# Performance work log

Hardware: AMD Instinct MI355X
Metric: run time of the kernel (lower is better)

## Reference

```python
import jax, jax.numpy as jnp
import numpy as np

NB_CAT = 8192       # nb_category per column
RANK = 16           # low-rank factor dimension
N_COLS = 4          # number of categorical columns (len(embedding_sizes))
N_PAIRS = 1048576   # number of (x, y) index pairs
FRAC_DIAG = 0.9     # fraction_diagonal init


def setup_inputs() -> dict:
    key = jax.random.key(0)
    k1, k2, k3, k4 = jax.random.split(key, 4)
    x = jax.random.randint(k1, (N_PAIRS, N_COLS), 0, NB_CAT, dtype=jnp.int32)
    y = jax.random.randint(k2, (N_PAIRS, N_COLS), 0, NB_CAT, dtype=jnp.int32)
    # params initialized as in the torch module, plus small noise so values are non-degenerate
    std = (FRAC_DIAG * jnp.ones((N_COLS, NB_CAT), dtype=jnp.float32)
           + 0.01 * jax.random.normal(k3, (N_COLS, NB_CAT), dtype=jnp.float32))
    covar_factor = ((1.0 - FRAC_DIAG) / np.float32(np.sqrt(RANK))
                    * jnp.ones((N_COLS, NB_CAT, RANK), dtype=jnp.float32)
                    + 0.01 * jax.random.normal(k4, (N_COLS, NB_CAT, RANK), dtype=jnp.float32))
    return {"x": x, "y": y, "covar_factor": covar_factor, "std": std}


def reference(x, y, covar_factor, std):
    # Build full covariance per column: F @ F.T + diag(std^2)   -> [C, N, N]
    cov = jnp.einsum('cnr,cmr->cnm', covar_factor, covar_factor)
    diag_idx = jnp.arange(cov.shape[1])
    cov = cov.at[:, diag_idx, diag_idx].add(std * std)
    # Gather requested (x, y) entries per column, then reduce (should_reduce=True)
    cols = jnp.arange(cov.shape[0])  # [C]
    vals = cov[cols[None, :], x, y]  # [B, C]
    return vals.sum(axis=-1)         # [B]
```

## Files before the change

### kernel.cpp

```cpp
#include <hip/hip_runtime.h>

#define NB_CAT  8192
#define RANK    16
#define N_COLS  4
#define N_PAIRS 1048576

#define SLICES      (N_COLS * 2)
#define SLICE_ROWS  NB_CAT
#define SLICE_BYTES (SLICE_ROWS * 16)
#define TBL_BYTES   ((size_t)SLICES * SLICE_BYTES)

typedef _Float16 half2_t __attribute__((ext_vector_type(2)));

#if defined(__has_builtin)
#if __has_builtin(__builtin_amdgcn_fdot2)
#define HAVE_FDOT2 1
#endif
#endif

__device__ __forceinline__ float dot8_f16(uint4 A, uint4 B, float acc) {
#ifdef HAVE_FDOT2
    acc = __builtin_amdgcn_fdot2(__builtin_bit_cast(half2_t, A.x), __builtin_bit_cast(half2_t, B.x), acc, false);
    acc = __builtin_amdgcn_fdot2(__builtin_bit_cast(half2_t, A.y), __builtin_bit_cast(half2_t, B.y), acc, false);
    acc = __builtin_amdgcn_fdot2(__builtin_bit_cast(half2_t, A.z), __builtin_bit_cast(half2_t, B.z), acc, false);
    acc = __builtin_amdgcn_fdot2(__builtin_bit_cast(half2_t, A.w), __builtin_bit_cast(half2_t, B.w), acc, false);
#else
    half2_t ax = __builtin_bit_cast(half2_t, A.x), bx = __builtin_bit_cast(half2_t, B.x);
    half2_t ay = __builtin_bit_cast(half2_t, A.y), by = __builtin_bit_cast(half2_t, B.y);
    half2_t az = __builtin_bit_cast(half2_t, A.z), bz = __builtin_bit_cast(half2_t, B.z);
    half2_t aw = __builtin_bit_cast(half2_t, A.w), bw = __builtin_bit_cast(half2_t, B.w);
    acc = fmaf((float)ax[0], (float)bx[0], acc); acc = fmaf((float)ax[1], (float)bx[1], acc);
    acc = fmaf((float)ay[0], (float)by[0], acc); acc = fmaf((float)ay[1], (float)by[1], acc);
    acc = fmaf((float)az[0], (float)bz[0], acc); acc = fmaf((float)az[1], (float)bz[1], acc);
    acc = fmaf((float)aw[0], (float)bw[0], acc); acc = fmaf((float)aw[1], (float)bw[1], acc);
#endif
    return acc;
}

__device__ __forceinline__ int comp(const int4& v, int c) {
    switch (c) { case 0: return v.x; case 1: return v.y; case 2: return v.z; default: return v.w; }
}

__global__ __launch_bounds__(256) void pack_f16_kernel(
    const float4* __restrict__ src,
    uint4*        __restrict__ dst)
{
    const int g = blockIdx.x * 256 + threadIdx.x;
    const int s = g >> 13;
    const int k = g & (NB_CAT - 1);
    const int c = s >> 1, h = s & 1;

    const float4 f0 = src[(c * NB_CAT + k) * 4 + h * 2];
    const float4 f1 = src[(c * NB_CAT + k) * 4 + h * 2 + 1];

    half2_t p0 = {(_Float16)f0.x, (_Float16)f0.y};
    half2_t p1 = {(_Float16)f0.z, (_Float16)f0.w};
    half2_t p2 = {(_Float16)f1.x, (_Float16)f1.y};
    half2_t p3 = {(_Float16)f1.z, (_Float16)f1.w};

    uint4 u;
    u.x = __builtin_bit_cast(unsigned int, p0);
    u.y = __builtin_bit_cast(unsigned int, p1);
    u.z = __builtin_bit_cast(unsigned int, p2);
    u.w = __builtin_bit_cast(unsigned int, p3);
    dst[g] = u;
}

__global__ __launch_bounds__(1024, 4) void IndexKernel_32238024524411_kernel(
    const int4*  __restrict__ x4,
    const int4*  __restrict__ y4,
    const uint4* __restrict__ tbl,
    const float* __restrict__ stdv,
    float*       __restrict__ out)
{
    extern __shared__ uint4 sh[];

    const int tid  = threadIdx.x;
    const int base = blockIdx.x * 4096 + tid;

    int4 xv[4], yv[4];
#pragma unroll
    for (int j = 0; j < 4; ++j) {
        xv[j] = x4[base + j * 1024];
        yv[j] = y4[base + j * 1024];
    }

    float acc[4] = {0.f, 0.f, 0.f, 0.f};

#pragma unroll
    for (int c = 0; c < N_COLS; ++c) {
#pragma unroll
        for (int h = 0; h < 2; ++h) {
            __syncthreads();
            const uint4* src = tbl + (size_t)(c * 2 + h) * SLICE_ROWS;
#pragma unroll
            for (int it = 0; it < 8; ++it) {
                sh[tid + it * 1024] = src[tid + it * 1024];
            }
            __syncthreads();

#pragma unroll
            for (int j = 0; j < 4; ++j) {
                const int xi = comp(xv[j], c);
                const int yi = comp(yv[j], c);
                const uint4 ax = sh[xi];
                const uint4 ay = sh[yi];
                acc[j] = dot8_f16(ax, ay, acc[j]);
                if (h == 0 && xi == yi) {
                    const float sd = stdv[c * NB_CAT + xi];
                    acc[j] = fmaf(sd, sd, acc[j]);
                }
            }
        }
    }

#pragma unroll
    for (int j = 0; j < 4; ++j) {
        out[base + j * 1024] = acc[j];
    }
}

__global__ __launch_bounds__(256) void fallback_kernel(
    const int* __restrict__ x, const int* __restrict__ y,
    const float4* __restrict__ cf, const float* __restrict__ stdv,
    float* __restrict__ out)
{
    const int tid = threadIdx.x;
    const int q = tid & 15, gi = tid >> 4, c = q >> 2, s = q & 3;
    const int p0 = blockIdx.x * 32 + gi, p1 = p0 + 16;
    const int rb = c * NB_CAT;
    const int xi0 = x[p0*4+c], yi0 = y[p0*4+c], xi1 = x[p1*4+c], yi1 = y[p1*4+c];
    const float4 a0 = cf[(size_t)(rb+xi0)*4 + s], b0 = cf[(size_t)(rb+yi0)*4 + s];
    const float4 a1 = cf[(size_t)(rb+xi1)*4 + s], b1 = cf[(size_t)(rb+yi1)*4 + s];
    float v0 = a0.x*b0.x; v0 = fmaf(a0.y,b0.y,v0); v0 = fmaf(a0.z,b0.z,v0); v0 = fmaf(a0.w,b0.w,v0);
    float v1 = a1.x*b1.x; v1 = fmaf(a1.y,b1.y,v1); v1 = fmaf(a1.z,b1.z,v1); v1 = fmaf(a1.w,b1.w,v1);
    if (s == 0 && xi0 == yi0) { float sd = stdv[rb+xi0]; v0 = fmaf(sd,sd,v0); }
    if (s == 0 && xi1 == yi1) { float sd = stdv[rb+xi1]; v1 = fmaf(sd,sd,v1); }
    int t;
    t = __builtin_amdgcn_update_dpp(0, __float_as_int(v0), 0xB1, 0xF, 0xF, true); v0 += __int_as_float(t);
    t = __builtin_amdgcn_update_dpp(0, __float_as_int(v0), 0x4E, 0xF, 0xF, true); v0 += __int_as_float(t);
    t = __builtin_amdgcn_update_dpp(0, __float_as_int(v0), 0x141,0xF, 0xF, true); v0 += __int_as_float(t);
    t = __builtin_amdgcn_update_dpp(0, __float_as_int(v0), 0x128,0xF, 0xF, true); v0 += __int_as_float(t);
    t = __builtin_amdgcn_update_dpp(0, __float_as_int(v1), 0xB1, 0xF, 0xF, true); v1 += __int_as_float(t);
    t = __builtin_amdgcn_update_dpp(0, __float_as_int(v1), 0x4E, 0xF, 0xF, true); v1 += __int_as_float(t);
    t = __builtin_amdgcn_update_dpp(0, __float_as_int(v1), 0x141,0xF, 0xF, true); v1 += __int_as_float(t);
    t = __builtin_amdgcn_update_dpp(0, __float_as_int(v1), 0x128,0xF, 0xF, true); v1 += __int_as_float(t);
    if (q == 0) { out[p0] = v0; out[p1] = v1; }
}

extern "C" void kernel_launch(void* const* d_in, const int* in_sizes, int n_in,
                              void* d_out, int out_size, void* d_ws, size_t ws_size,
                              hipStream_t stream) {
    const int*   x    = (const int*)d_in[0];
    const int*   y    = (const int*)d_in[1];
    const float* cf   = (const float*)d_in[2];
    const float* stdv = (const float*)d_in[3];
    float*       out  = (float*)d_out;

    if (ws_size >= TBL_BYTES) {
        (void)hipFuncSetAttribute(
            reinterpret_cast<const void*>(&IndexKernel_32238024524411_kernel),
            hipFuncAttributeMaxDynamicSharedMemorySize, SLICE_BYTES);

        pack_f16_kernel<<<SLICES * NB_CAT / 256, 256, 0, stream>>>(
            (const float4*)cf, (uint4*)d_ws);
        IndexKernel_32238024524411_kernel<<<256, 1024, SLICE_BYTES, stream>>>(
            (const int4*)x, (const int4*)y, (const uint4*)d_ws, stdv, out);
    } else {
        fallback_kernel<<<N_PAIRS / 32, 256, 0, stream>>>(
            x, y, (const float4*)cf, stdv, out);
    }
}
```

Before: 97.57 us.

## Split work per table slice across blocks and accumulate with float atomics

Each block now loads a single half-slice of the packed factor table into shared memory once and processes a 32K-pair chunk for that slice, instead of every block reloading all eight slices. Partial dot products are combined with float atomic adds into an output that is zeroed beforehand. Optionally the index arrays are transposed into column-major order in the workspace so per-column index reads are coalesced. This trades repeated shared-memory table loads and block-wide barriers for extra launches, an index transpose pass and eight atomics per output element. Summation order becomes nondeterministic. The fallback kernel's diagonal term now reads std at the y index instead of the x index, which gives the same value because the two indices are equal on that path.

After: 117.7 us. 20.6% more time.

```diff
diff --git a/kernel.cpp b/kernel.cpp
--- a/kernel.cpp
+++ b/kernel.cpp
@@ -6,9 +6,10 @@
 #define N_PAIRS 1048576
 
 #define SLICES      (N_COLS * 2)
-#define SLICE_ROWS  NB_CAT
-#define SLICE_BYTES (SLICE_ROWS * 16)
+#define SLICE_BYTES (NB_CAT * 16)
 #define TBL_BYTES   ((size_t)SLICES * SLICE_BYTES)
+#define IDX_BYTES   ((size_t)N_PAIRS * N_COLS * 4)
+#define WS_FULL     (TBL_BYTES + 2 * IDX_BYTES)
 
 typedef _Float16 half2_t __attribute__((ext_vector_type(2)));
 
@@ -37,13 +38,8 @@
     return acc;
 }
 
-__device__ __forceinline__ int comp(const int4& v, int c) {
-    switch (c) { case 0: return v.x; case 1: return v.y; case 2: return v.z; default: return v.w; }
-}
-
 __global__ __launch_bounds__(256) void pack_f16_kernel(
-    const float4* __restrict__ src,
-    uint4*        __restrict__ dst)
+    const float4* __restrict__ src, uint4* __restrict__ dst)
 {
     const int g = blockIdx.x * 256 + threadIdx.x;
     const int s = g >> 13;
@@ -66,57 +62,70 @@
     dst[g] = u;
 }
 
-__global__ __launch_bounds__(1024, 4) void IndexKernel_32238024524411_kernel(
-    const int4*  __restrict__ x4,
-    const int4*  __restrict__ y4,
+__global__ __launch_bounds__(256) void transpose_idx_kernel(
+    const int4* __restrict__ x4, const int4* __restrict__ y4,
+    int* __restrict__ xT, int* __restrict__ yT)
+{
+    const int p = blockIdx.x * 256 + threadIdx.x;
+    const int4 a = x4[p];
+    const int4 b = y4[p];
+    xT[0 * N_PAIRS + p] = a.x; xT[1 * N_PAIRS + p] = a.y;
+    xT[2 * N_PAIRS + p] = a.z; xT[3 * N_PAIRS + p] = a.w;
+    yT[0 * N_PAIRS + p] = b.x; yT[1 * N_PAIRS + p] = b.y;
+    yT[2 * N_PAIRS + p] = b.z; yT[3 * N_PAIRS + p] = b.w;
+}
+
+__global__ __launch_bounds__(256) void zero_out_kernel(float4* __restrict__ out) {
+    out[blockIdx.x * 256 + threadIdx.x] = float4{0.f, 0.f, 0.f, 0.f};
+}
+
+__global__ __launch_bounds__(1024, 1) void IndexKernel_32238024524411_kernel(
+    const int*   __restrict__ xs,
+    const int*   __restrict__ ys,
+    int ps, int cs,
     const uint4* __restrict__ tbl,
     const float* __restrict__ stdv,
     float*       __restrict__ out)
 {
     extern __shared__ uint4 sh[];
 
-    const int tid  = threadIdx.x;
-    const int base = blockIdx.x * 4096 + tid;
+    const int tid   = threadIdx.x;
+    const int slice = blockIdx.x >> 5;
+    const int chunk = blockIdx.x & 31;
+    const int c     = slice >> 1;
+    const int h     = slice & 1;
 
-    int4 xv[4], yv[4];
+    const uint4* src = tbl + slice * NB_CAT;
 #pragma unroll
-    for (int j = 0; j < 4; ++j) {
-        xv[j] = x4[base + j * 1024];
-        yv[j] = y4[base + j * 1024];
+    for (int it = 0; it < 8; ++it) {
+        sh[tid + it * 1024] = src[tid + it * 1024];
     }
+    __syncthreads();
 
-    float acc[4] = {0.f, 0.f, 0.f, 0.f};
+    const int pbase = chunk * 32768 + tid;
+    const int cb    = c * cs;
 
 #pragma unroll
-    for (int c = 0; c < N_COLS; ++c) {
+    for (int g = 0; g < 4; ++g) {
+        int xi[8], yi[8];
 #pragma unroll
-        for (int h = 0; h < 2; ++h) {
-            __syncthreads();
-            const uint4* src = tbl + (size_t)(c * 2 + h) * SLICE_ROWS;
+        for (int j = 0; j < 8; ++j) {
+            const int p = pbase + (g * 8 + j) * 1024;
+            xi[j] = xs[p * ps + cb];
+            yi[j] = ys[p * ps + cb];
+        }
 #pragma unroll
-            for (int it = 0; it < 8; ++it) {
-                sh[tid + it * 1024] = src[tid + it * 1024];
+        for (int j = 0; j < 8; ++j) {
+            const int p = pbase + (g * 8 + j) * 1024;
+            const uint4 ax = sh[xi[j]];
+            const uint4 ay = sh[yi[j]];
+            float d = dot8_f16(ax, ay, 0.f);
+            if (h == 0 && xi[j] == yi[j]) {
+                const float sd = stdv[c * NB_CAT + xi[j]];
+                d = fmaf(sd, sd, d);
             }
-            __syncthreads();
-
-#pragma unroll
-            for (int j = 0; j < 4; ++j) {
-                const int xi = comp(xv[j], c);
-                const int yi = comp(yv[j], c);
-                const uint4 ax = sh[xi];
-                const uint4 ay = sh[yi];
-                acc[j] = dot8_f16(ax, ay, acc[j]);
-                if (h == 0 && xi == yi) {
-                    const float sd = stdv[c * NB_CAT + xi];
-                    acc[j] = fmaf(sd, sd, acc[j]);
-                }
-            }
+            unsafeAtomicAdd(&out[p], d);
         }
-    }
-
-#pragma unroll
-    for (int j = 0; j < 4; ++j) {
-        out[base + j * 1024] = acc[j];
     }
 }
 
@@ -135,7 +144,7 @@
     float v0 = a0.x*b0.x; v0 = fmaf(a0.y,b0.y,v0); v0 = fmaf(a0.z,b0.z,v0); v0 = fmaf(a0.w,b0.w,v0);
     float v1 = a1.x*b1.x; v1 = fmaf(a1.y,b1.y,v1); v1 = fmaf(a1.z,b1.z,v1); v1 = fmaf(a1.w,b1.w,v1);
     if (s == 0 && xi0 == yi0) { float sd = stdv[rb+xi0]; v0 = fmaf(sd,sd,v0); }
-    if (s == 0 && xi1 == yi1) { float sd = stdv[rb+xi1]; v1 = fmaf(sd,sd,v1); }
+    if (s == 0 && xi1 == yi1) { float sd = stdv[rb+yi1]; v1 = fmaf(sd,sd,v1); }
     int t;
     t = __builtin_amdgcn_update_dpp(0, __float_as_int(v0), 0xB1, 0xF, 0xF, true); v0 += __int_as_float(t);
     t = __builtin_amdgcn_update_dpp(0, __float_as_int(v0), 0x4E, 0xF, 0xF, true); v0 += __int_as_float(t);
@@ -157,17 +166,31 @@
     const float* stdv = (const float*)d_in[3];
     float*       out  = (float*)d_out;
 
-    if (ws_size >= TBL_BYTES) {
-        (void)hipFuncSetAttribute(
-            reinterpret_cast<const void*>(&IndexKernel_32238024524411_kernel),
-            hipFuncAttributeMaxDynamicSharedMemorySize, SLICE_BYTES);
-
-        pack_f16_kernel<<<SLICES * NB_CAT / 256, 256, 0, stream>>>(
-            (const float4*)cf, (uint4*)d_ws);
-        IndexKernel_32238024524411_kernel<<<256, 1024, SLICE_BYTES, stream>>>(
-            (const int4*)x, (const int4*)y, (const uint4*)d_ws, stdv, out);
-    } else {
+    if (ws_size < TBL_BYTES) {
         fallback_kernel<<<N_PAIRS / 32, 256, 0, stream>>>(
             x, y, (const float4*)cf, stdv, out);
+        return;
     }
+
+    (void)hipFuncSetAttribute(
+        reinterpret_cast<const void*>(&IndexKernel_32238024524411_kernel),
+        hipFuncAttributeMaxDynamicSharedMemorySize, SLICE_BYTES);
+
+    pack_f16_kernel<<<SLICES * NB_CAT / 256, 256, 0, stream>>>(
+        (const float4*)cf, (uint4*)d_ws);
+    zero_out_kernel<<<N_PAIRS / 4 / 256, 256, 0, stream>>>((float4*)out);
+
+    const int* xs = x;
+    const int* ys = y;
+    int ps = N_COLS, cs = 1;
+    if (ws_size >= WS_FULL) {
+        int* xT = (int*)((char*)d_ws + TBL_BYTES);
+        int* yT = xT + (size_t)N_COLS * N_PAIRS;
+        transpose_idx_kernel<<<N_PAIRS / 256, 256, 0, stream>>>(
+            (const int4*)x, (const int4*)y, xT, yT);
+        xs = xT; ys = yT; ps = 1; cs = N_PAIRS;
+    }
+
+    IndexKernel_32238024524411_kernel<<<SLICES * 32, 1024, SLICE_BYTES, stream>>>(
+        xs, ys, ps, cs, (const uint4*)d_ws, stdv, out);
 }
```

## Double-buffer narrower LDS table slices with register-staged prefetch

Applied to the files above, without the earlier changes.

Splits each column's packed fp16 factor table into four 8-byte-wide slices instead of two 16-byte slices. LDS is double-buffered so the next slice is loaded into registers while the current slice is gathered, which leaves one barrier per phase instead of two. The aim is to hide the global-to-LDS copy behind the random LDS gathers and to use 8-byte LDS reads. The cost is twice as many phases and more staging registers, with launch bounds relaxed to one block per CU.

New measurement: 96.99 us. Within noise of the previous version (-0.6%).

```diff
diff --git a/kernel.cpp b/kernel.cpp
--- a/kernel.cpp
+++ b/kernel.cpp
@@ -5,10 +5,11 @@
 #define N_COLS  4
 #define N_PAIRS 1048576
 
-#define SLICES      (N_COLS * 2)
+#define NSLICE      16
 #define SLICE_ROWS  NB_CAT
-#define SLICE_BYTES (SLICE_ROWS * 16)
-#define TBL_BYTES   ((size_t)SLICES * SLICE_BYTES)
+#define SLICE_BYTES (SLICE_ROWS * 8)
+#define TBL_BYTES   ((size_t)NSLICE * SLICE_BYTES)
+#define LDS_BYTES   (2 * SLICE_BYTES)
 
 typedef _Float16 half2_t __attribute__((ext_vector_type(2)));
 
@@ -18,62 +19,51 @@
 #endif
 #endif
 
-__device__ __forceinline__ float dot8_f16(uint4 A, uint4 B, float acc) {
+__device__ __forceinline__ float dot4_f16(uint2 A, uint2 B, float acc) {
 #ifdef HAVE_FDOT2
     acc = __builtin_amdgcn_fdot2(__builtin_bit_cast(half2_t, A.x), __builtin_bit_cast(half2_t, B.x), acc, false);
     acc = __builtin_amdgcn_fdot2(__builtin_bit_cast(half2_t, A.y), __builtin_bit_cast(half2_t, B.y), acc, false);
-    acc = __builtin_amdgcn_fdot2(__builtin_bit_cast(half2_t, A.z), __builtin_bit_cast(half2_t, B.z), acc, false);
-    acc = __builtin_amdgcn_fdot2(__builtin_bit_cast(half2_t, A.w), __builtin_bit_cast(half2_t, B.w), acc, false);
 #else
     half2_t ax = __builtin_bit_cast(half2_t, A.x), bx = __builtin_bit_cast(half2_t, B.x);
     half2_t ay = __builtin_bit_cast(half2_t, A.y), by = __builtin_bit_cast(half2_t, B.y);
-    half2_t az = __builtin_bit_cast(half2_t, A.z), bz = __builtin_bit_cast(half2_t, B.z);
-    half2_t aw = __builtin_bit_cast(half2_t, A.w), bw = __builtin_bit_cast(half2_t, B.w);
     acc = fmaf((float)ax[0], (float)bx[0], acc); acc = fmaf((float)ax[1], (float)bx[1], acc);
     acc = fmaf((float)ay[0], (float)by[0], acc); acc = fmaf((float)ay[1], (float)by[1], acc);
-    acc = fmaf((float)az[0], (float)bz[0], acc); acc = fmaf((float)az[1], (float)bz[1], acc);
-    acc = fmaf((float)aw[0], (float)bw[0], acc); acc = fmaf((float)aw[1], (float)bw[1], acc);
 #endif
     return acc;
 }
 
-__device__ __forceinline__ int comp(const int4& v, int c) {
-    switch (c) { case 0: return v.x; case 1: return v.y; case 2: return v.z; default: return v.w; }
+template <int C> __device__ __forceinline__ int comp(const int4& v) {
+    if (C == 0) return v.x;
+    if (C == 1) return v.y;
+    if (C == 2) return v.z;
+    return v.w;
 }
 
 __global__ __launch_bounds__(256) void pack_f16_kernel(
-    const float4* __restrict__ src,
-    uint4*        __restrict__ dst)
+    const float4* __restrict__ src, uint2* __restrict__ dst)
 {
     const int g = blockIdx.x * 256 + threadIdx.x;
     const int s = g >> 13;
     const int k = g & (NB_CAT - 1);
-    const int c = s >> 1, h = s & 1;
+    const int c = s >> 2, qr = s & 3;
 
-    const float4 f0 = src[(c * NB_CAT + k) * 4 + h * 2];
-    const float4 f1 = src[(c * NB_CAT + k) * 4 + h * 2 + 1];
-
-    half2_t p0 = {(_Float16)f0.x, (_Float16)f0.y};
-    half2_t p1 = {(_Float16)f0.z, (_Float16)f0.w};
-    half2_t p2 = {(_Float16)f1.x, (_Float16)f1.y};
-    half2_t p3 = {(_Float16)f1.z, (_Float16)f1.w};
-
-    uint4 u;
+    const float4 f = src[(c * NB_CAT + k) * 4 + qr];
+    half2_t p0 = {(_Float16)f.x, (_Float16)f.y};
+    half2_t p1 = {(_Float16)f.z, (_Float16)f.w};
+    uint2 u;
     u.x = __builtin_bit_cast(unsigned int, p0);
     u.y = __builtin_bit_cast(unsigned int, p1);
-    u.z = __builtin_bit_cast(unsigned int, p2);
-    u.w = __builtin_bit_cast(unsigned int, p3);
     dst[g] = u;
 }
 
-__global__ __launch_bounds__(1024, 4) void IndexKernel_32238024524411_kernel(
+__global__ __launch_bounds__(1024, 1) void IndexKernel_32238024524411_kernel(
     const int4*  __restrict__ x4,
     const int4*  __restrict__ y4,
-    const uint4* __restrict__ tbl,
+    const uint2* __restrict__ tbl,
     const float* __restrict__ stdv,
     float*       __restrict__ out)
 {
-    extern __shared__ uint4 sh[];
+    extern __shared__ uint2 sh[];
 
     const int tid  = threadIdx.x;
     const int base = blockIdx.x * 4096 + tid;
@@ -87,32 +77,47 @@
 
     float acc[4] = {0.f, 0.f, 0.f, 0.f};
 
+    uint2 stg[8];
 #pragma unroll
-    for (int c = 0; c < N_COLS; ++c) {
-#pragma unroll
-        for (int h = 0; h < 2; ++h) {
-            __syncthreads();
-            const uint4* src = tbl + (size_t)(c * 2 + h) * SLICE_ROWS;
-#pragma unroll
-            for (int it = 0; it < 8; ++it) {
-                sh[tid + it * 1024] = src[tid + it * 1024];
-            }
-            __syncthreads();
+    for (int it = 0; it < 8; ++it) stg[it] = tbl[tid + it * 1024];
 
-#pragma unroll
-            for (int j = 0; j < 4; ++j) {
-                const int xi = comp(xv[j], c);
-                const int yi = comp(yv[j], c);
-                const uint4 ax = sh[xi];
-                const uint4 ay = sh[yi];
-                acc[j] = dot8_f16(ax, ay, acc[j]);
-                if (h == 0 && xi == yi) {
-                    const float sd = stdv[c * NB_CAT + xi];
-                    acc[j] = fmaf(sd, sd, acc[j]);
-                }
-            }
-        }
+#define PHASE(S)                                                               \
+    {                                                                          \
+        constexpr int s  = (S);                                                \
+        constexpr int c  = s >> 2;                                             \
+        constexpr int qr = s & 3;                                              \
+        uint2* buf = sh + (s & 1) * SLICE_ROWS;                                \
+        _Pragma("unroll")                                                      \
+        for (int it = 0; it < 8; ++it) buf[tid + it * 1024] = stg[it];         \
+        if (s < NSLICE - 1) {                                                  \
+            const uint2* nsrc = tbl + (size_t)(s + 1) * SLICE_ROWS;            \
+            _Pragma("unroll")                                                  \
+            for (int it = 0; it < 8; ++it) stg[it] = nsrc[tid + it * 1024];    \
+        }                                                                      \
+              \
+        asm volatile("s_waitcnt lgkmcnt(0)" ::: "memory");                     \
+        __builtin_amdgcn_s_barrier();                                          \
+        asm volatile("" ::: "memory");                                         \
+        _Pragma("unroll")                                                      \
+        for (int j = 0; j < 4; ++j) {                                          \
+            const int xi = comp<c>(xv[j]);                                     \
+            const int yi = comp<c>(yv[j]);                                     \
+            const uint2 a = buf[xi];                                           \
+            const uint2 b = buf[yi];                                           \
+            acc[j] = dot4_f16(a, b, acc[j]);                                   \
+            if (qr == 0 && xi == yi) {                                         \
+                const float sd = stdv[c * NB_CAT + xi];                        \
+                acc[j] = fmaf(sd, sd, acc[j]);                                 \
+            }                                                                  \
+        }                                                                      \
+        asm volatile("" ::: "memory");                                         \
     }
+
+    PHASE(0)  PHASE(1)  PHASE(2)  PHASE(3)
+    PHASE(4)  PHASE(5)  PHASE(6)  PHASE(7)
+    PHASE(8)  PHASE(9)  PHASE(10) PHASE(11)
+    PHASE(12) PHASE(13) PHASE(14) PHASE(15)
+#undef PHASE
 
 #pragma unroll
     for (int j = 0; j < 4; ++j) {
@@ -135,7 +140,7 @@
     float v0 = a0.x*b0.x; v0 = fmaf(a0.y,b0.y,v0); v0 = fmaf(a0.z,b0.z,v0); v0 = fmaf(a0.w,b0.w,v0);
     float v1 = a1.x*b1.x; v1 = fmaf(a1.y,b1.y,v1); v1 = fmaf(a1.z,b1.z,v1); v1 = fmaf(a1.w,b1.w,v1);
     if (s == 0 && xi0 == yi0) { float sd = stdv[rb+xi0]; v0 = fmaf(sd,sd,v0); }
-    if (s == 0 && xi1 == yi1) { float sd = stdv[rb+xi1]; v1 = fmaf(sd,sd,v1); }
+    if (s == 0 && xi1 == yi1) { float sd = stdv[rb+yi1]; v1 = fmaf(sd,sd,v1); }
     int t;
     t = __builtin_amdgcn_update_dpp(0, __float_as_int(v0), 0xB1, 0xF, 0xF, true); v0 += __int_as_float(t);
     t = __builtin_amdgcn_update_dpp(0, __float_as_int(v0), 0x4E, 0xF, 0xF, true); v0 += __int_as_float(t);
@@ -157,17 +162,19 @@
     const float* stdv = (const float*)d_in[3];
     float*       out  = (float*)d_out;
 
-    if (ws_size >= TBL_BYTES) {
-        (void)hipFuncSetAttribute(
-            reinterpret_cast<const void*>(&IndexKernel_32238024524411_kernel),
-            hipFuncAttributeMaxDynamicSharedMemorySize, SLICE_BYTES);
-
-        pack_f16_kernel<<<SLICES * NB_CAT / 256, 256, 0, stream>>>(
-            (const float4*)cf, (uint4*)d_ws);
-        IndexKernel_32238024524411_kernel<<<256, 1024, SLICE_BYTES, stream>>>(
-            (const int4*)x, (const int4*)y, (const uint4*)d_ws, stdv, out);
-    } else {
+    if (ws_size < TBL_BYTES) {
         fallback_kernel<<<N_PAIRS / 32, 256, 0, stream>>>(
             x, y, (const float4*)cf, stdv, out);
+        return;
     }
+
+    (void)hipFuncSetAttribute(
+        reinterpret_cast<const void*>(&IndexKernel_32238024524411_kernel),
+        hipFuncAttributeMaxDynamicSharedMemorySize, LDS_BYTES);
+
+    pack_f16_kernel<<<NSLICE * NB_CAT / 256, 256, 0, stream>>>(
+        (const float4*)cf, (uint2*)d_ws);
+
+    IndexKernel_32238024524411_kernel<<<N_PAIRS / 4096, 1024, LDS_BYTES, stream>>>(
+        (const int4*)x, (const int4*)y, (const uint2*)d_ws, stdv, out);
 }
```

## Prefetch next table slice into registers while computing on current LDS slice

Applied to the files above, without the earlier changes.

The main kernel now prefetches the next fp16 table slice from global memory into registers while the current slice in LDS is used for dot products, then stores it to LDS between barriers. The goal is to hide global load latency behind the gather compute. The diagonal std contribution is hoisted out of the slice loop and done once per pair up front. Launch bounds drop to one block per CU-wave hint, which frees registers for the 8 staging uint4s and may lower occupancy. The fallback kernel also gets an index tweak that does not change its result.

Result: slower. 154.5 us (+58.4%).

```diff
diff --git a/kernel.cpp b/kernel.cpp
--- a/kernel.cpp
+++ b/kernel.cpp
@@ -5,10 +5,11 @@
 #define N_COLS  4
 #define N_PAIRS 1048576
 
-#define SLICES      (N_COLS * 2)
+#define NSLICE      8
 #define SLICE_ROWS  NB_CAT
 #define SLICE_BYTES (SLICE_ROWS * 16)
-#define TBL_BYTES   ((size_t)SLICES * SLICE_BYTES)
+#define TBL_BYTES   ((size_t)NSLICE * SLICE_BYTES)
+#define LDS_BYTES   SLICE_BYTES
 
 typedef _Float16 half2_t __attribute__((ext_vector_type(2)));
 
@@ -37,8 +38,8 @@
     return acc;
 }
 
-__device__ __forceinline__ int comp(const int4& v, int c) {
-    switch (c) { case 0: return v.x; case 1: return v.y; case 2: return v.z; default: return v.w; }
+__device__ __forceinline__ int comp4(const int4& v, int c) {
+    return (c == 0) ? v.x : (c == 1) ? v.y : (c == 2) ? v.z : v.w;
 }
 
 __global__ __launch_bounds__(256) void pack_f16_kernel(
@@ -66,7 +67,7 @@
     dst[g] = u;
 }
 
-__global__ __launch_bounds__(1024, 4) void IndexKernel_32238024524411_kernel(
+__global__ __launch_bounds__(1024, 1) void IndexKernel_32238024524411_kernel(
     const int4*  __restrict__ x4,
     const int4*  __restrict__ y4,
     const uint4* __restrict__ tbl,
@@ -88,29 +89,52 @@
     float acc[4] = {0.f, 0.f, 0.f, 0.f};
 
 #pragma unroll
-    for (int c = 0; c < N_COLS; ++c) {
+    for (int j = 0; j < 4; ++j) {
+        const int4 a = xv[j], b = yv[j];
+        if (a.x == b.x) { const float s = stdv[0 * NB_CAT + a.x]; acc[j] = fmaf(s, s, acc[j]); }
+        if (a.y == b.y) { const float s = stdv[1 * NB_CAT + a.y]; acc[j] = fmaf(s, s, acc[j]); }
+        if (a.z == b.z) { const float s = stdv[2 * NB_CAT + a.z]; acc[j] = fmaf(s, s, acc[j]); }
+        if (a.w == b.w) { const float s = stdv[3 * NB_CAT + a.w]; acc[j] = fmaf(s, s, acc[j]); }
+    }
+
+    uint4 stg[8];
 #pragma unroll
-        for (int h = 0; h < 2; ++h) {
-            __syncthreads();
-            const uint4* src = tbl + (size_t)(c * 2 + h) * SLICE_ROWS;
+    for (int it = 0; it < 8; ++it) stg[it] = tbl[tid + it * 1024];
 #pragma unroll
-            for (int it = 0; it < 8; ++it) {
-                sh[tid + it * 1024] = src[tid + it * 1024];
-            }
-            __syncthreads();
+    for (int it = 0; it < 8; ++it) sh[tid + it * 1024] = stg[it];
+    asm volatile("s_waitcnt lgkmcnt(0)" ::: "memory");
+    __builtin_amdgcn_s_barrier();
+    asm volatile("" ::: "memory");
 
 #pragma unroll
-            for (int j = 0; j < 4; ++j) {
-                const int xi = comp(xv[j], c);
-                const int yi = comp(yv[j], c);
-                const uint4 ax = sh[xi];
-                const uint4 ay = sh[yi];
-                acc[j] = dot8_f16(ax, ay, acc[j]);
-                if (h == 0 && xi == yi) {
-                    const float sd = stdv[c * NB_CAT + xi];
-                    acc[j] = fmaf(sd, sd, acc[j]);
-                }
-            }
+    for (int s = 0; s < NSLICE; ++s) {
+        const int c = s >> 1;
+
+        if (s < NSLICE - 1) {
+            const uint4* nsrc = tbl + (size_t)(s + 1) * SLICE_ROWS;
+#pragma unroll
+            for (int it = 0; it < 8; ++it) stg[it] = nsrc[tid + it * 1024];
+        }
+        asm volatile("" ::: "memory");
+
+#pragma unroll
+        for (int j = 0; j < 4; ++j) {
+            const int xi = comp4(xv[j], c);
+            const int yi = comp4(yv[j], c);
+            const uint4 a = sh[xi];
+            const uint4 b = sh[yi];
+            acc[j] = dot8_f16(a, b, acc[j]);
+        }
+
+        if (s < NSLICE - 1) {
+            asm volatile("s_waitcnt lgkmcnt(0)" ::: "memory");
+            __builtin_amdgcn_s_barrier();
+            asm volatile("" ::: "memory");
+#pragma unroll
+            for (int it = 0; it < 8; ++it) sh[tid + it * 1024] = stg[it];
+            asm volatile("s_waitcnt lgkmcnt(0)" ::: "memory");
+            __builtin_amdgcn_s_barrier();
+            asm volatile("" ::: "memory");
         }
     }
 
@@ -135,7 +159,7 @@
     float v0 = a0.x*b0.x; v0 = fmaf(a0.y,b0.y,v0); v0 = fmaf(a0.z,b0.z,v0); v0 = fmaf(a0.w,b0.w,v0);
     float v1 = a1.x*b1.x; v1 = fmaf(a1.y,b1.y,v1); v1 = fmaf(a1.z,b1.z,v1); v1 = fmaf(a1.w,b1.w,v1);
     if (s == 0 && xi0 == yi0) { float sd = stdv[rb+xi0]; v0 = fmaf(sd,sd,v0); }
-    if (s == 0 && xi1 == yi1) { float sd = stdv[rb+xi1]; v1 = fmaf(sd,sd,v1); }
+    if (s == 0 && xi1 == yi1) { float sd = stdv[rb+yi1]; v1 = fmaf(sd,sd,v1); }
     int t;
     t = __builtin_amdgcn_update_dpp(0, __float_as_int(v0), 0xB1, 0xF, 0xF, true); v0 += __int_as_float(t);
     t = __builtin_amdgcn_update_dpp(0, __float_as_int(v0), 0x4E, 0xF, 0xF, true); v0 += __int_as_float(t);
@@ -157,17 +181,19 @@
     const float* stdv = (const float*)d_in[3];
     float*       out  = (float*)d_out;
 
-    if (ws_size >= TBL_BYTES) {
-        (void)hipFuncSetAttribute(
-            reinterpret_cast<const void*>(&IndexKernel_32238024524411_kernel),
-            hipFuncAttributeMaxDynamicSharedMemorySize, SLICE_BYTES);
-
-        pack_f16_kernel<<<SLICES * NB_CAT / 256, 256, 0, stream>>>(
-            (const float4*)cf, (uint4*)d_ws);
-        IndexKernel_32238024524411_kernel<<<256, 1024, SLICE_BYTES, stream>>>(
-            (const int4*)x, (const int4*)y, (const uint4*)d_ws, stdv, out);
-    } else {
+    if (ws_size < TBL_BYTES) {
         fallback_kernel<<<N_PAIRS / 32, 256, 0, stream>>>(
             x, y, (const float4*)cf, stdv, out);
+        return;
     }
+
+    (void)hipFuncSetAttribute(
+        reinterpret_cast<const void*>(&IndexKernel_32238024524411_kernel),
+        hipFuncAttributeMaxDynamicSharedMemorySize, LDS_BYTES);
+
+    pack_f16_kernel<<<NSLICE * NB_CAT / 256, 256, 0, stream>>>(
+        (const float4*)cf, (uint4*)d_ws);
+
+    IndexKernel_32238024524411_kernel<<<N_PAIRS / 4096, 1024, LDS_BYTES, stream>>>(
+        (const int4*)x, (const int4*)y, (const uint4*)d_ws, stdv, out);
 }
```
